# Kernel optimization log

Measured on AMD Instinct MI355X. Metric: run time of the kernel, lower is better.

## Reference

```python
import jax, jax.numpy as jnp
import numpy as np

NUM_HEADS = 8
SLOPE = 8.0  # relative_bias_slope
NEG_SLOPE = 0.2  # LeakyReLU


def _rel_coords_table(L):
    # RelativePosEmb: table is (n+1, n+1, 1) with n = L-1; row/col 0 are zeros
    n = L - 1
    coords = jnp.linspace(-SLOPE / 2, SLOPE / 2, n)
    rel = coords[None, :] - coords[:, None]  # [n, n]
    tab = jnp.sign(rel) * jnp.log2(jnp.abs(rel) + 1.0) / np.log2(SLOPE + 1.0)
    full = jnp.zeros((L, L), dtype=tab.dtype).at[1:, 1:].set(tab)
    return full[..., None]  # [L, L, 1]


def setup_inputs() -> dict:
    key = jax.random.key(0)
    ks = jax.random.split(key, 7)
    B, L, C, inter = 16, 1024, 512, 64
    x = jax.random.normal(ks[0], (B, L, C), dtype=jnp.float32)
    attn_mask = jax.random.randint(ks[1], (B, L - 1), 0, 2) > 0
    W_qkv = jax.random.normal(ks[2], (C, 3 * C), dtype=jnp.float32) * 0.02
    W1 = jax.random.normal(ks[3], (1, inter), dtype=jnp.float32) * 0.5
    b1 = jax.random.normal(ks[4], (inter,), dtype=jnp.float32) * 0.1
    W2 = jax.random.normal(ks[5], (inter, NUM_HEADS), dtype=jnp.float32) * 0.1
    W_out = jax.random.normal(ks[6], (C, C), dtype=jnp.float32) * 0.02
    return {"x": x, "attn_mask": attn_mask, "W_qkv": W_qkv, "W1": W1,
            "b1": b1, "W2": W2, "W_out": W_out}


def reference(x, attn_mask, W_qkv, W1, b1, W2, W_out):
    B, L, C = x.shape
    H = NUM_HEADS
    d = C // H
    # QKV projection (no bias)
    qkv = (x @ W_qkv).reshape(B, L, 3, H, d)
    q = qkv[:, :, 0].transpose(0, 2, 1, 3)  # [B,H,L,d]
    k = qkv[:, :, 1].transpose(0, 2, 1, 3)
    v = qkv[:, :, 2].transpose(0, 2, 1, 3)
    # relative position bias via tiny MLP: [L,L,1] -> [L,L,H]
    tab = _rel_coords_table(L)
    h = jax.nn.leaky_relu(tab @ W1 + b1, NEG_SLOPE)
    rel_bias = (h @ W2).transpose(2, 0, 1)[None]  # [1,H,L,L]
    # mask: prepend always-true column, broadcast over query dim
    m = jnp.concatenate([jnp.ones((B, 1), dtype=bool), attn_mask], axis=1)  # [B,L]
    bias = jnp.where(m[:, None, None, :], rel_bias, -jnp.inf)  # [B,H,L,L]
    # math SDPA: softmax(q k^T / sqrt(d) + bias) v
    scores = jnp.einsum('bhld,bhmd->bhlm', q, k) * (d ** -0.5) + bias
    attn = jax.nn.softmax(scores, axis=-1)
    out = jnp.einsum('bhlm,bhmd->bhld', attn, v)
    out = out.transpose(0, 2, 1, 3).reshape(B, L, C)
    return out @ W_out
```

## Files before the change

kernel.cpp:

```cpp
#include <hip/hip_runtime.h>
#include <hip/hip_bf16.h>

typedef short s16x8 __attribute__((ext_vector_type(8)));
typedef float f32x4 __attribute__((ext_vector_type(4)));
typedef float f32x16 __attribute__((ext_vector_type(16)));
typedef unsigned int u32;
typedef unsigned int u32x4 __attribute__((ext_vector_type(4)));
typedef unsigned short u16x4 __attribute__((ext_vector_type(4)));
typedef unsigned long long u64;

#define LOG2E 1.4426950408889634f
#define QSCALE 0.18033688011112042f
#define NEG_BIG -3.0e38f

#define PKS(dst, a, b) asm("v_cvt_pk_bf16_f32 %0, %1, %2" : "=v"(dst) : "v"(a), "v"(b))
#define SWP(x, y) asm("v_permlane32_swap_b32 %0, %1" : "+v"(x), "+v"(y))

__device__ __forceinline__ unsigned short f2b(float f) {
    unsigned int u = __float_as_uint(f);
    unsigned int r = (u + 0x7fffu + ((u >> 16) & 1u)) >> 16;
    return (unsigned short)r;
}

__device__ __forceinline__ void g2l16(const void* g, void* l) {
    __builtin_amdgcn_global_load_lds(
        (const __attribute__((address_space(1))) unsigned int*)(g),
        (__attribute__((address_space(3))) unsigned int*)(l), 16, 0, 0);
}

__global__ __launch_bounds__(256) void k_prepw(const float* __restrict__ Wqkv,
                                               unsigned short* __restrict__ wqkvT,
                                               const float* __restrict__ Wout,
                                               unsigned short* __restrict__ woutT,
                                               const float* __restrict__ W1,
                                               const float* __restrict__ b1,
                                               const float* __restrict__ W2,
                                               float* __restrict__ btab) {
    int bid = blockIdx.x, tid = threadIdx.x;
    {
        int idx = bid * 256 + tid;
        int k = idx & 511, n = idx >> 9;
        wqkvT[idx] = f2b(Wqkv[(long)k * 1536 + n]);
    }
    if (bid < 1024) {
        int idx = bid * 256 + tid;
        int k = idx & 511, n = idx >> 9;
        woutT[idx] = f2b(Wout[(long)k * 512 + n]);
    }
    if (bid >= 3064) {
        int idx = (bid - 3064) * 256 + tid;
        if (idx <= 2045) {
            float t = 0.0f;
            if (idx != 2045) {
                float r = (float)(idx - 1022) * (8.0f / 1022.0f);
                float sg = (r > 0.f) ? 1.0f : ((r < 0.f) ? -1.0f : 0.0f);
                t = sg * log2f(fabsf(r) + 1.0f) * 0.3154648767971406f;
            }
            float acc[8] = {0, 0, 0, 0, 0, 0, 0, 0};
            float accc[8] = {0, 0, 0, 0, 0, 0, 0, 0};
            for (int j = 0; j < 64; ++j) {
                float hj = t * W1[j] + b1[j];
                hj = (hj > 0.f) ? hj : 0.2f * hj;
                float hc = b1[j];
                hc = (hc > 0.f) ? hc : 0.2f * hc;
                #pragma unroll
                for (int h = 0; h < 8; ++h) {
                    acc[h] += hj * W2[j * 8 + h];
                    accc[h] += hc * W2[j * 8 + h];
                }
            }
            #pragma unroll
            for (int h = 0; h < 8; ++h) {
                btab[h * 4096 + idx] = acc[h] * LOG2E - 8.0f;
                btab[h * 4096 + 2048 + idx] = accc[h] * LOG2E - 8.0f;
            }
        }
    }
}

template <int MODE>
__global__ __launch_bounds__(256) void k_gemm(const float* __restrict__ Af,
                                              const unsigned short* __restrict__ A16,
                                              const unsigned short* __restrict__ BT,
                                              int M, int N,
                                              unsigned short* __restrict__ Qp,
                                              unsigned short* __restrict__ Kp,
                                              unsigned short* __restrict__ VTp,
                                              float* __restrict__ Cout) {
    __shared__ __align__(16) unsigned short As[2][128 * 32];
    __shared__ __align__(16) unsigned short Bs[2][128 * 32];
    constexpr int NX = (MODE == 0) ? 12 : 4;
    constexpr int NWG = (MODE == 0) ? 1536 : 512;
    int lid = blockIdx.y * NX + blockIdx.x;
    int tile = (lid & 7) * (NWG >> 3) + (lid >> 3);
    int m0 = (tile / NX) * 128, n0 = (tile % NX) * 128;
    int tid = threadIdx.x;
    int wave = tid >> 6, lane = tid & 63, lr = lane & 15, g = lane >> 4;
    int wr = wave >> 1, wc = wave & 1;
    f32x4 acc[4][4] = {};
    const float* Af0 = Af + (long)(m0 + (tid >> 2)) * 512 + (tid & 3) * 8;
    const float* Af1 = Af0 + 64 * 512;
    const char* Ab = (const char*)A16 + (long)(m0 + (tid >> 2)) * 1024 + (tid & 3) * 16;
    const char* Bb = (const char*)BT + (long)(n0 + (tid >> 2)) * 1024 + (tid & 3) * 16;

    if (MODE == 0) {
        f32x4 a0 = *(const f32x4*)(Af0);
        f32x4 a1 = *(const f32x4*)(Af0 + 4);
        f32x4 a2 = *(const f32x4*)(Af1);
        f32x4 a3 = *(const f32x4*)(Af1 + 4);
        u32 w0, w1, w2, w3;
        PKS(w0, a0.x, a0.y); PKS(w1, a0.z, a0.w);
        PKS(w2, a1.x, a1.y); PKS(w3, a1.z, a1.w);
        *(u32x4*)((char*)As[0] + tid * 16) = u32x4{w0, w1, w2, w3};
        PKS(w0, a2.x, a2.y); PKS(w1, a2.z, a2.w);
        PKS(w2, a3.x, a3.y); PKS(w3, a3.z, a3.w);
        *(u32x4*)((char*)As[0] + 4096 + tid * 16) = u32x4{w0, w1, w2, w3};
    } else {
        g2l16(Ab, (char*)As[0] + wave * 1024);
        g2l16(Ab + 65536, (char*)As[0] + 4096 + wave * 1024);
    }
    g2l16(Bb, (char*)Bs[0] + wave * 1024);
    g2l16(Bb + 65536, (char*)Bs[0] + 4096 + wave * 1024);
    __syncthreads();

    for (int kt = 0; kt < 16; ++kt) {
        int cur = kt & 1;
        int nxt = cur ^ 1;
        f32x4 na0, na1, na2, na3;
        if (kt < 15) {
            if (MODE == 0) {
                na0 = *(const f32x4*)(Af0 + (kt + 1) * 32);
                na1 = *(const f32x4*)(Af0 + (kt + 1) * 32 + 4);
                na2 = *(const f32x4*)(Af1 + (kt + 1) * 32);
                na3 = *(const f32x4*)(Af1 + (kt + 1) * 32 + 4);
            } else {
                g2l16(Ab + (kt + 1) * 64, (char*)As[nxt] + wave * 1024);
                g2l16(Ab + 65536 + (kt + 1) * 64, (char*)As[nxt] + 4096 + wave * 1024);
            }
            g2l16(Bb + (kt + 1) * 64, (char*)Bs[nxt] + wave * 1024);
            g2l16(Bb + 65536 + (kt + 1) * 64, (char*)Bs[nxt] + 4096 + wave * 1024);
        }
        s16x8 av[4], bv[4];
        #pragma unroll
        for (int f = 0; f < 4; ++f) {
            av[f] = *(const s16x8*)((char*)As[cur] + (wr * 64 + f * 16 + lr) * 64 + g * 16);
            bv[f] = *(const s16x8*)((char*)Bs[cur] + (wc * 64 + f * 16 + lr) * 64 + g * 16);
        }
        __builtin_amdgcn_s_setprio(1);
        #pragma unroll
        for (int fi = 0; fi < 4; ++fi)
            #pragma unroll
            for (int fj = 0; fj < 4; ++fj)
                acc[fi][fj] = __builtin_amdgcn_mfma_f32_16x16x32_bf16(bv[fj], av[fi], acc[fi][fj], 0, 0, 0);
        __builtin_amdgcn_s_setprio(0);
        if (MODE == 0 && kt < 15) {
            u32 w0, w1, w2, w3;
            PKS(w0, na0.x, na0.y); PKS(w1, na0.z, na0.w);
            PKS(w2, na1.x, na1.y); PKS(w3, na1.z, na1.w);
            *(u32x4*)((char*)As[nxt] + tid * 16) = u32x4{w0, w1, w2, w3};
            PKS(w0, na2.x, na2.y); PKS(w1, na2.z, na2.w);
            PKS(w2, na3.x, na3.y); PKS(w3, na3.z, na3.w);
            *(u32x4*)((char*)As[nxt] + 4096 + tid * 16) = u32x4{w0, w1, w2, w3};
        }
        __syncthreads();
    }
    #pragma unroll
    for (int fi = 0; fi < 4; ++fi) {
        int gm = m0 + wr * 64 + fi * 16 + lr;
        if (MODE == 0) {
            int bq = gm >> 10, lp = gm & 1023;
            int kvt = lp >> 6, kvl = lp & 63;
            #pragma unroll
            for (int fj = 0; fj < 4; ++fj) {
                int col0 = n0 + wc * 64 + fj * 16 + g * 4;
                int sec = col0 >> 9, c0 = col0 & 511, h = c0 >> 6, dd0 = c0 & 63;
                int bh = bq * 8 + h;
                float v0 = acc[fi][fj][0], v1 = acc[fi][fj][1];
                float v2 = acc[fi][fj][2], v3 = acc[fi][fj][3];
                if (sec == 0) {
                    u32 w0, w1;
                    float q0 = v0 * QSCALE, q1 = v1 * QSCALE, q2 = v2 * QSCALE, q3 = v3 * QSCALE;
                    PKS(w0, q0, q1); PKS(w1, q2, q3);
                    *(uint2*)(Qp + (long)(bh * 1024 + lp) * 64 + dd0) = make_uint2(w0, w1);
                } else if (sec == 1) {
                    u32 w0, w1;
                    PKS(w0, v0, v1); PKS(w1, v2, v3);
                    long off = (long)bh * 65536 + kvt * 4096 + (kvl >> 5) * 2048 +
                               (dd0 >> 4) * 512 + ((((dd0 >> 3) & 1) << 5) + (kvl & 31)) * 8 + (dd0 & 7);
                    *(uint2*)(Kp + off) = make_uint2(w0, w1);
                } else {
                    long off = (long)bh * 65536 + kvt * 4096 + (dd0 >> 5) * 2048 +
                               (kvl >> 4) * 512 + ((((kvl >> 3) & 1) << 5) + (dd0 & 31)) * 8 + (kvl & 7);
                    VTp[off] = f2b(v0);
                    VTp[off + 8] = f2b(v1);
                    VTp[off + 16] = f2b(v2);
                    VTp[off + 24] = f2b(v3);
                }
            }
        } else {
            #pragma unroll
            for (int fj = 0; fj < 4; ++fj) {
                int col0 = n0 + wc * 64 + fj * 16 + g * 4;
                *(f32x4*)(Cout + (long)gm * N + col0) = acc[fi][fj];
            }
        }
    }
}

#define ATT_STAGE(MTT) do { \
    char* Kn_ = smem + ((MTT) % 3) * 16384; \
    g2l16(Kg + (MTT) * 8192 + tid * 16, Kn_ + wave * 1024); \
    g2l16(Vg + (MTT) * 8192 + tid * 16, Kn_ + 8192 + wave * 1024); \
  } while (0)

#define ATT_PV(VPTR) do { \
    __builtin_amdgcn_s_setprio(1); \
    o0 = __builtin_amdgcn_mfma_f32_32x32x16_bf16(*(const s16x8*)((VPTR) + lx), Pc0, o0, 0, 0, 0); \
    o0 = __builtin_amdgcn_mfma_f32_32x32x16_bf16(*(const s16x8*)((VPTR) + 1024 + lx), Pc1, o0, 0, 0, 0); \
    o0 = __builtin_amdgcn_mfma_f32_32x32x16_bf16(*(const s16x8*)((VPTR) + 2048 + lx), Pc2, o0, 0, 0, 0); \
    o0 = __builtin_amdgcn_mfma_f32_32x32x16_bf16(*(const s16x8*)((VPTR) + 3072 + lx), Pc3, o0, 0, 0, 0); \
    o1 = __builtin_amdgcn_mfma_f32_32x32x16_bf16(*(const s16x8*)((VPTR) + 4096 + lx), Pc0, o1, 0, 0, 0); \
    o1 = __builtin_amdgcn_mfma_f32_32x32x16_bf16(*(const s16x8*)((VPTR) + 5120 + lx), Pc1, o1, 0, 0, 0); \
    o1 = __builtin_amdgcn_mfma_f32_32x32x16_bf16(*(const s16x8*)((VPTR) + 6144 + lx), Pc2, o1, 0, 0, 0); \
    o1 = __builtin_amdgcn_mfma_f32_32x32x16_bf16(*(const s16x8*)((VPTR) + 7168 + lx), Pc3, o1, 0, 0, 0); \
    __builtin_amdgcn_s_setprio(0); \
  } while (0)

#define ATT_ITER(MT) do { \
    if ((MT) + 1 < 16) ATT_STAGE((MT) + 1); \
    char* Kl = smem + ((MT) % 3) * 16384; \
    int ib = (MT) * 64 - l + 1022; \
    float b0[16], b1v[16]; \
    { \
        const float* bq = bp + ib + 4 * hi; \
        _Pragma("unroll") \
        for (int k = 0; k < 4; ++k) { \
            f32x4 va = *(const f32x4*)(bq + 8 * k); \
            f32x4 vb = *(const f32x4*)(bq + 32 + 8 * k); \
            b0[4 * k + 0] = va.x; b0[4 * k + 1] = va.y; \
            b0[4 * k + 2] = va.z; b0[4 * k + 3] = va.w; \
            b1v[4 * k + 0] = vb.x; b1v[4 * k + 1] = vb.y; \
            b1v[4 * k + 2] = vb.z; b1v[4 * k + 3] = vb.w; \
        } \
    } \
    f32x16 s0 = {}, s1 = {}; \
    __builtin_amdgcn_s_setprio(1); \
    s0 = __builtin_amdgcn_mfma_f32_32x32x16_bf16(*(const s16x8*)(Kl + lx), qf0, s0, 0, 0, 0); \
    s0 = __builtin_amdgcn_mfma_f32_32x32x16_bf16(*(const s16x8*)(Kl + 1024 + lx), qf1, s0, 0, 0, 0); \
    s0 = __builtin_amdgcn_mfma_f32_32x32x16_bf16(*(const s16x8*)(Kl + 2048 + lx), qf2, s0, 0, 0, 0); \
    s0 = __builtin_amdgcn_mfma_f32_32x32x16_bf16(*(const s16x8*)(Kl + 3072 + lx), qf3, s0, 0, 0, 0); \
    s1 = __builtin_amdgcn_mfma_f32_32x32x16_bf16(*(const s16x8*)(Kl + 4096 + lx), qf0, s1, 0, 0, 0); \
    s1 = __builtin_amdgcn_mfma_f32_32x32x16_bf16(*(const s16x8*)(Kl + 5120 + lx), qf1, s1, 0, 0, 0); \
    s1 = __builtin_amdgcn_mfma_f32_32x32x16_bf16(*(const s16x8*)(Kl + 6144 + lx), qf2, s1, 0, 0, 0); \
    s1 = __builtin_amdgcn_mfma_f32_32x32x16_bf16(*(const s16x8*)(Kl + 7168 + lx), qf3, s1, 0, 0, 0); \
    __builtin_amdgcn_s_setprio(0); \
    if ((MT) > 0) { \
        char* Vp = smem + (((MT) + 2) % 3) * 16384 + 8192; \
        ATT_PV(Vp); \
    } \
    u64 mb = *(const u64*)(smem + 49152 + (MT) * 8); \
    u32 wm0 = (u32)(mb >> (4 * hi)); \
    u32 wm1 = (u32)(mb >> (32 + 4 * hi)); \
    if ((MT) == 0 && hi == 0) b0[0] = c2; \
    _Pragma("unroll") \
    for (int r = 0; r < 16; ++r) { \
        int pos = (r & 3) + 8 * (r >> 2); \
        s0[r] = ((wm0 >> pos) & 1) ? s0[r] + b0[r] : NEG_BIG; \
        s1[r] = ((wm1 >> pos) & 1) ? s1[r] + b1v[r] : NEG_BIG; \
    } \
    _Pragma("unroll") \
    for (int r = 0; r < 16; ++r) s0[r] = __builtin_amdgcn_exp2f(s0[r]); \
    _Pragma("unroll") \
    for (int r = 0; r < 16; ++r) s1[r] = __builtin_amdgcn_exp2f(s1[r]); \
    { \
        float u0 = s0[0] + s0[1], u1 = s0[2] + s0[3], u2 = s0[4] + s0[5], u3 = s0[6] + s0[7]; \
        float u4 = s0[8] + s0[9], u5 = s0[10] + s0[11], u6 = s0[12] + s0[13], u7 = s0[14] + s0[15]; \
        float v0 = s1[0] + s1[1], v1 = s1[2] + s1[3], v2 = s1[4] + s1[5], v3 = s1[6] + s1[7]; \
        float v4 = s1[8] + s1[9], v5 = s1[10] + s1[11], v6 = s1[12] + s1[13], v7 = s1[14] + s1[15]; \
        u0 += u1; u2 += u3; u4 += u5; u6 += u7; \
        v0 += v1; v2 += v3; v4 += v5; v6 += v7; \
        u0 += u2; u4 += u6; v0 += v2; v4 += v6; \
        float ts = (u0 + u4) + (v0 + v4); \
        ts += __shfl_xor(ts, 32); \
        Ss += ts; \
    } \
    { \
        u32 x, y, x2, y2; \
        union { u32 w[4]; s16x8 v; } pt; \
        PKS(x, s0[0], s0[1]);  PKS(y, s0[4], s0[5]);  SWP(x, y); \
        PKS(x2, s0[2], s0[3]); PKS(y2, s0[6], s0[7]); SWP(x2, y2); \
        pt.w[0] = x; pt.w[1] = x2; pt.w[2] = y; pt.w[3] = y2; Pc0 = pt.v; \
        PKS(x, s0[8], s0[9]);   PKS(y, s0[12], s0[13]);  SWP(x, y); \
        PKS(x2, s0[10], s0[11]); PKS(y2, s0[14], s0[15]); SWP(x2, y2); \
        pt.w[0] = x; pt.w[1] = x2; pt.w[2] = y; pt.w[3] = y2; Pc1 = pt.v; \
        PKS(x, s1[0], s1[1]);  PKS(y, s1[4], s1[5]);  SWP(x, y); \
        PKS(x2, s1[2], s1[3]); PKS(y2, s1[6], s1[7]); SWP(x2, y2); \
        pt.w[0] = x; pt.w[1] = x2; pt.w[2] = y; pt.w[3] = y2; Pc2 = pt.v; \
        PKS(x, s1[8], s1[9]);   PKS(y, s1[12], s1[13]);  SWP(x, y); \
        PKS(x2, s1[10], s1[11]); PKS(y2, s1[14], s1[15]); SWP(x2, y2); \
        pt.w[0] = x; pt.w[1] = x2; pt.w[2] = y; pt.w[3] = y2; Pc3 = pt.v; \
    } \
    __syncthreads(); \
  } while (0)

__global__ __launch_bounds__(512, 2) void k_attn(const unsigned short* __restrict__ Q,
                                                 const unsigned short* __restrict__ Kb,
                                                 const unsigned short* __restrict__ VT,
                                                 const int* __restrict__ mask,
                                                 const float* __restrict__ btab,
                                                 unsigned short* __restrict__ AO) {
    __shared__ __align__(16) char smem[56320];
    int lid = blockIdx.x;
    int wg = (lid & 7) * 64 + (lid >> 3);
    int qt = wg & 3, bh = wg >> 2;
    int b = bh >> 3, h = bh & 7;
    int tid = threadIdx.x;
    int wave = tid >> 6, lane = tid & 63;
    int q = lane & 31, hi = lane >> 5;
    int l = qt * 256 + wave * 32 + q;
    const float* bt = btab + h * 4096;
    float c2 = bt[2045];
    const float* bp = bt + ((l == 0) ? 2048 : 0);

    const char* Kg = (const char*)Kb + (long)bh * 131072;
    const char* Vg = (const char*)VT + (long)bh * 131072;

    if (tid < 16) {
        const int* mrow = mask + b * 1023;
        u64 bits = 0;
        for (int j = 0; j < 64; ++j) {
            int kv = tid * 64 + j;
            int bit = (kv == 0) ? 1 : (mrow[kv - 1] != 0);
            bits |= (u64)bit << j;
        }
        *(u64*)(smem + 49152 + tid * 8) = bits;
    }

    const char* Qrow = (const char*)Q + ((long)bh * 1024 + l) * 128;
    s16x8 qf0 = *(const s16x8*)(Qrow + 0 * 32 + hi * 16);
    s16x8 qf1 = *(const s16x8*)(Qrow + 1 * 32 + hi * 16);
    s16x8 qf2 = *(const s16x8*)(Qrow + 2 * 32 + hi * 16);
    s16x8 qf3 = *(const s16x8*)(Qrow + 3 * 32 + hi * 16);

    f32x16 o0 = {}, o1 = {};
    float Ss = 0.f;
    int lx = lane * 16;
    s16x8 Pc0 = {}, Pc1 = {}, Pc2 = {}, Pc3 = {};

    ATT_STAGE(0);
    __syncthreads();

    ATT_ITER(0);  ATT_ITER(1);  ATT_ITER(2);  ATT_ITER(3);
    ATT_ITER(4);  ATT_ITER(5);  ATT_ITER(6);  ATT_ITER(7);
    ATT_ITER(8);  ATT_ITER(9);  ATT_ITER(10); ATT_ITER(11);
    ATT_ITER(12); ATT_ITER(13); ATT_ITER(14); ATT_ITER(15);

    {
        char* Vp = smem + 0 * 16384 + 8192;
        ATT_PV(Vp);
    }
    __syncthreads();

    float inv = 1.0f / Ss;
    char* Ob = smem;
    int qloc = wave * 32 + q;
    #pragma unroll
    for (int j = 0; j < 4; ++j) {
        u32 wa, wb;
        float va0 = o0[j * 4 + 0] * inv, va1 = o0[j * 4 + 1] * inv;
        float va2 = o0[j * 4 + 2] * inv, va3 = o0[j * 4 + 3] * inv;
        PKS(wa, va0, va1); PKS(wb, va2, va3);
        int d0 = 8 * j + 4 * hi;
        *(uint2*)(Ob + qloc * 128 + ((d0 * 2) ^ ((qloc & 7) << 4))) = make_uint2(wa, wb);
    }
    #pragma unroll
    for (int j = 0; j < 4; ++j) {
        u32 wa, wb;
        float va0 = o1[j * 4 + 0] * inv, va1 = o1[j * 4 + 1] * inv;
        float va2 = o1[j * 4 + 2] * inv, va3 = o1[j * 4 + 3] * inv;
        PKS(wa, va0, va1); PKS(wb, va2, va3);
        int d0 = 32 + 8 * j + 4 * hi;
        *(uint2*)(Ob + qloc * 128 + ((d0 * 2) ^ ((qloc & 7) << 4))) = make_uint2(wa, wb);
    }
    __syncthreads();
    long gb = (long)(b * 1024 + qt * 256) * 512 + h * 64;
    #pragma unroll
    for (int p = 0; p < 4; ++p) {
        int qr = p * 64 + (tid >> 3);
        int ss = tid & 7;
        u32x4 vv = *(const u32x4*)(Ob + qr * 128 + ((ss * 16) ^ ((qr & 7) << 4)));
        *(u32x4*)((char*)AO + (gb + (long)qr * 512 + ss * 8) * 2) = vv;
    }
}


extern "C" void kernel_launch(void* const* d_in, const int* in_sizes, int n_in,
                              void* d_out, int out_size, void* d_ws, size_t ws_size,
                              hipStream_t stream) {
    const float* x    = (const float*)d_in[0];
    const int*   mask = (const int*)d_in[1];
    const float* Wqkv = (const float*)d_in[2];
    const float* W1   = (const float*)d_in[3];
    const float* b1   = (const float*)d_in[4];
    const float* W2   = (const float*)d_in[5];
    const float* Wout = (const float*)d_in[6];
    float* out = (float*)d_out;
    char* ws = (char*)d_ws;

    unsigned short* wqkvT = (unsigned short*)(ws + 16777216);
    unsigned short* woutT = (unsigned short*)(ws + 18350080);
    unsigned short* Qb    = (unsigned short*)(ws + 18874368);
    unsigned short* Kb    = (unsigned short*)(ws + 35651584);
    unsigned short* VTb   = (unsigned short*)(ws + 52428800);
    unsigned short* AOb   = (unsigned short*)(ws + 69206016);
    float* btab           = (float*)(ws + 85983232);
    if (ws_size < 86114304) return;

    k_prepw<<<3072, 256, 0, stream>>>(Wqkv, wqkvT, Wout, woutT, W1, b1, W2, btab);
    k_gemm<0><<<dim3(12, 128), 256, 0, stream>>>(x, nullptr, wqkvT, 16384, 1536, Qb, Kb, VTb, nullptr);
    k_attn<<<512, 512, 0, stream>>>(Qb, Kb, VTb, mask, btab, AOb);
    k_gemm<1><<<dim3(4, 128), 256, 0, stream>>>(nullptr, AOb, woutT, 16384, 512, nullptr, nullptr, nullptr, out);
}
```

Baseline: 142.5 us.

## Software-pipeline attention loop: overlap next-tile QK MFMA with previous tile softmax

Restructures the attention inner loop so the QK^T MFMAs for tile MT are issued before the softmax, bias/mask and PV of tile MT-1, using double-buffered score registers (sA/sB). The aim is to hide the exp2/bias/pack VALU work behind matrix-core work from the next tile instead of serializing QK then softmax within each iteration. It adds two more 16-wide f32 register arrays, which raises register pressure at launch bounds 512x2 and could cause spills. The 3-stage LDS buffer must still hold V of tile MT-1 while K of MT+1 is loaded.

```diff
diff --git a/kernel.cpp b/kernel.cpp
--- a/kernel.cpp
+++ b/kernel.cpp
@@ -213,6 +213,23 @@
     g2l16(Vg + (MTT) * 8192 + tid * 16, Kn_ + 8192 + wave * 1024); \
   } while (0)
 
+#define ATT_QK(MT, S0, S1) do { \
+    if ((MT) + 1 < 16) ATT_STAGE((MT) + 1); \
+    char* Kl = smem + ((MT) % 3) * 16384; \
+    f32x16 t0_ = {}, t1_ = {}; \
+    __builtin_amdgcn_s_setprio(1); \
+    t0_ = __builtin_amdgcn_mfma_f32_32x32x16_bf16(*(const s16x8*)(Kl + lx), qf0, t0_, 0, 0, 0); \
+    t0_ = __builtin_amdgcn_mfma_f32_32x32x16_bf16(*(const s16x8*)(Kl + 1024 + lx), qf1, t0_, 0, 0, 0); \
+    t0_ = __builtin_amdgcn_mfma_f32_32x32x16_bf16(*(const s16x8*)(Kl + 2048 + lx), qf2, t0_, 0, 0, 0); \
+    t0_ = __builtin_amdgcn_mfma_f32_32x32x16_bf16(*(const s16x8*)(Kl + 3072 + lx), qf3, t0_, 0, 0, 0); \
+    t1_ = __builtin_amdgcn_mfma_f32_32x32x16_bf16(*(const s16x8*)(Kl + 4096 + lx), qf0, t1_, 0, 0, 0); \
+    t1_ = __builtin_amdgcn_mfma_f32_32x32x16_bf16(*(const s16x8*)(Kl + 5120 + lx), qf1, t1_, 0, 0, 0); \
+    t1_ = __builtin_amdgcn_mfma_f32_32x32x16_bf16(*(const s16x8*)(Kl + 6144 + lx), qf2, t1_, 0, 0, 0); \
+    t1_ = __builtin_amdgcn_mfma_f32_32x32x16_bf16(*(const s16x8*)(Kl + 7168 + lx), qf3, t1_, 0, 0, 0); \
+    __builtin_amdgcn_s_setprio(0); \
+    S0 = t0_; S1 = t1_; \
+  } while (0)
+
 #define ATT_PV(VPTR) do { \
     __builtin_amdgcn_s_setprio(1); \
     o0 = __builtin_amdgcn_mfma_f32_32x32x16_bf16(*(const s16x8*)((VPTR) + lx), Pc0, o0, 0, 0, 0); \
@@ -226,10 +243,8 @@
     __builtin_amdgcn_s_setprio(0); \
   } while (0)
 
-#define ATT_ITER(MT) do { \
-    if ((MT) + 1 < 16) ATT_STAGE((MT) + 1); \
-    char* Kl = smem + ((MT) % 3) * 16384; \
-    int ib = (MT) * 64 - l + 1022; \
+#define ATT_SM(MTP, S0, S1) do { \
+    int ib = (MTP) * 64 - l + 1022; \
     float b0[16], b1v[16]; \
     { \
         const float* bq = bp + ib + 4 * hi; \
@@ -243,40 +258,25 @@
             b1v[4 * k + 2] = vb.z; b1v[4 * k + 3] = vb.w; \
         } \
     } \
-    f32x16 s0 = {}, s1 = {}; \
-    __builtin_amdgcn_s_setprio(1); \
-    s0 = __builtin_amdgcn_mfma_f32_32x32x16_bf16(*(const s16x8*)(Kl + lx), qf0, s0, 0, 0, 0); \
-    s0 = __builtin_amdgcn_mfma_f32_32x32x16_bf16(*(const s16x8*)(Kl + 1024 + lx), qf1, s0, 0, 0, 0); \
-    s0 = __builtin_amdgcn_mfma_f32_32x32x16_bf16(*(const s16x8*)(Kl + 2048 + lx), qf2, s0, 0, 0, 0); \
-    s0 = __builtin_amdgcn_mfma_f32_32x32x16_bf16(*(const s16x8*)(Kl + 3072 + lx), qf3, s0, 0, 0, 0); \
-    s1 = __builtin_amdgcn_mfma_f32_32x32x16_bf16(*(const s16x8*)(Kl + 4096 + lx), qf0, s1, 0, 0, 0); \
-    s1 = __builtin_amdgcn_mfma_f32_32x32x16_bf16(*(const s16x8*)(Kl + 5120 + lx), qf1, s1, 0, 0, 0); \
-    s1 = __builtin_amdgcn_mfma_f32_32x32x16_bf16(*(const s16x8*)(Kl + 6144 + lx), qf2, s1, 0, 0, 0); \
-    s1 = __builtin_amdgcn_mfma_f32_32x32x16_bf16(*(const s16x8*)(Kl + 7168 + lx), qf3, s1, 0, 0, 0); \
-    __builtin_amdgcn_s_setprio(0); \
-    if ((MT) > 0) { \
-        char* Vp = smem + (((MT) + 2) % 3) * 16384 + 8192; \
-        ATT_PV(Vp); \
-    } \
-    u64 mb = *(const u64*)(smem + 49152 + (MT) * 8); \
+    u64 mb = *(const u64*)(smem + 49152 + (MTP) * 8); \
     u32 wm0 = (u32)(mb >> (4 * hi)); \
     u32 wm1 = (u32)(mb >> (32 + 4 * hi)); \
-    if ((MT) == 0 && hi == 0) b0[0] = c2; \
+    if ((MTP) == 0 && hi == 0) b0[0] = c2; \
     _Pragma("unroll") \
     for (int r = 0; r < 16; ++r) { \
         int pos = (r & 3) + 8 * (r >> 2); \
-        s0[r] = ((wm0 >> pos) & 1) ? s0[r] + b0[r] : NEG_BIG; \
-        s1[r] = ((wm1 >> pos) & 1) ? s1[r] + b1v[r] : NEG_BIG; \
+        S0[r] = ((wm0 >> pos) & 1) ? S0[r] + b0[r] : NEG_BIG; \
+        S1[r] = ((wm1 >> pos) & 1) ? S1[r] + b1v[r] : NEG_BIG; \
     } \
     _Pragma("unroll") \
-    for (int r = 0; r < 16; ++r) s0[r] = __builtin_amdgcn_exp2f(s0[r]); \
+    for (int r = 0; r < 16; ++r) S0[r] = __builtin_amdgcn_exp2f(S0[r]); \
     _Pragma("unroll") \
-    for (int r = 0; r < 16; ++r) s1[r] = __builtin_amdgcn_exp2f(s1[r]); \
+    for (int r = 0; r < 16; ++r) S1[r] = __builtin_amdgcn_exp2f(S1[r]); \
     { \
-        float u0 = s0[0] + s0[1], u1 = s0[2] + s0[3], u2 = s0[4] + s0[5], u3 = s0[6] + s0[7]; \
-        float u4 = s0[8] + s0[9], u5 = s0[10] + s0[11], u6 = s0[12] + s0[13], u7 = s0[14] + s0[15]; \
-        float v0 = s1[0] + s1[1], v1 = s1[2] + s1[3], v2 = s1[4] + s1[5], v3 = s1[6] + s1[7]; \
-        float v4 = s1[8] + s1[9], v5 = s1[10] + s1[11], v6 = s1[12] + s1[13], v7 = s1[14] + s1[15]; \
+        float u0 = S0[0] + S0[1], u1 = S0[2] + S0[3], u2 = S0[4] + S0[5], u3 = S0[6] + S0[7]; \
+        float u4 = S0[8] + S0[9], u5 = S0[10] + S0[11], u6 = S0[12] + S0[13], u7 = S0[14] + S0[15]; \
+        float v0 = S1[0] + S1[1], v1 = S1[2] + S1[3], v2 = S1[4] + S1[5], v3 = S1[6] + S1[7]; \
+        float v4 = S1[8] + S1[9], v5 = S1[10] + S1[11], v6 = S1[12] + S1[13], v7 = S1[14] + S1[15]; \
         u0 += u1; u2 += u3; u4 += u5; u6 += u7; \
         v0 += v1; v2 += v3; v4 += v5; v6 += v7; \
         u0 += u2; u4 += u6; v0 += v2; v4 += v6; \
@@ -287,19 +287,28 @@
     { \
         u32 x, y, x2, y2; \
         union { u32 w[4]; s16x8 v; } pt; \
-        PKS(x, s0[0], s0[1]);  PKS(y, s0[4], s0[5]);  SWP(x, y); \
-        PKS(x2, s0[2], s0[3]); PKS(y2, s0[6], s0[7]); SWP(x2, y2); \
+        PKS(x, S0[0], S0[1]);  PKS(y, S0[4], S0[5]);  SWP(x, y); \
+        PKS(x2, S0[2], S0[3]); PKS(y2, S0[6], S0[7]); SWP(x2, y2); \
         pt.w[0] = x; pt.w[1] = x2; pt.w[2] = y; pt.w[3] = y2; Pc0 = pt.v; \
-        PKS(x, s0[8], s0[9]);   PKS(y, s0[12], s0[13]);  SWP(x, y); \
-        PKS(x2, s0[10], s0[11]); PKS(y2, s0[14], s0[15]); SWP(x2, y2); \
+        PKS(x, S0[8], S0[9]);   PKS(y, S0[12], S0[13]);  SWP(x, y); \
+        PKS(x2, S0[10], S0[11]); PKS(y2, S0[14], S0[15]); SWP(x2, y2); \
         pt.w[0] = x; pt.w[1] = x2; pt.w[2] = y; pt.w[3] = y2; Pc1 = pt.v; \
-        PKS(x, s1[0], s1[1]);  PKS(y, s1[4], s1[5]);  SWP(x, y); \
-        PKS(x2, s1[2], s1[3]); PKS(y2, s1[6], s1[7]); SWP(x2, y2); \
+        PKS(x, S1[0], S1[1]);  PKS(y, S1[4], S1[5]);  SWP(x, y); \
+        PKS(x2, S1[2], S1[3]); PKS(y2, S1[6], S1[7]); SWP(x2, y2); \
         pt.w[0] = x; pt.w[1] = x2; pt.w[2] = y; pt.w[3] = y2; Pc2 = pt.v; \
-        PKS(x, s1[8], s1[9]);   PKS(y, s1[12], s1[13]);  SWP(x, y); \
-        PKS(x2, s1[10], s1[11]); PKS(y2, s1[14], s1[15]); SWP(x2, y2); \
+        PKS(x, S1[8], S1[9]);   PKS(y, S1[12], S1[13]);  SWP(x, y); \
+        PKS(x2, S1[10], S1[11]); PKS(y2, S1[14], S1[15]); SWP(x2, y2); \
         pt.w[0] = x; pt.w[1] = x2; pt.w[2] = y; pt.w[3] = y2; Pc3 = pt.v; \
     } \
+    { \
+        char* Vp_ = smem + ((MTP) % 3) * 16384 + 8192; \
+        ATT_PV(Vp_); \
+    } \
+  } while (0)
+
+#define ATT_IT(MT, SC0, SC1, SP0, SP1) do { \
+    ATT_QK(MT, SC0, SC1); \
+    ATT_SM((MT) - 1, SP0, SP1); \
     __syncthreads(); \
   } while (0)
 
@@ -346,19 +355,24 @@
     float Ss = 0.f;
     int lx = lane * 16;
     s16x8 Pc0 = {}, Pc1 = {}, Pc2 = {}, Pc3 = {};
+    f32x16 sA0, sA1, sB0, sB1;
 
     ATT_STAGE(0);
     __syncthreads();
 
-    ATT_ITER(0);  ATT_ITER(1);  ATT_ITER(2);  ATT_ITER(3);
-    ATT_ITER(4);  ATT_ITER(5);  ATT_ITER(6);  ATT_ITER(7);
-    ATT_ITER(8);  ATT_ITER(9);  ATT_ITER(10); ATT_ITER(11);
-    ATT_ITER(12); ATT_ITER(13); ATT_ITER(14); ATT_ITER(15);
-
-    {
-        char* Vp = smem + 0 * 16384 + 8192;
-        ATT_PV(Vp);
-    }
+    ATT_QK(0, sA0, sA1);
+    __syncthreads();
+
+    ATT_IT(1, sB0, sB1, sA0, sA1);   ATT_IT(2, sA0, sA1, sB0, sB1);
+    ATT_IT(3, sB0, sB1, sA0, sA1);   ATT_IT(4, sA0, sA1, sB0, sB1);
+    ATT_IT(5, sB0, sB1, sA0, sA1);   ATT_IT(6, sA0, sA1, sB0, sB1);
+    ATT_IT(7, sB0, sB1, sA0, sA1);   ATT_IT(8, sA0, sA1, sB0, sB1);
+    ATT_IT(9, sB0, sB1, sA0, sA1);   ATT_IT(10, sA0, sA1, sB0, sB1);
+    ATT_IT(11, sB0, sB1, sA0, sA1);  ATT_IT(12, sA0, sA1, sB0, sB1);
+    ATT_IT(13, sB0, sB1, sA0, sA1);  ATT_IT(14, sA0, sA1, sB0, sB1);
+    ATT_IT(15, sB0, sB1, sA0, sA1);
+
+    ATT_SM(15, sB0, sB1);
     __syncthreads();
 
     float inv = 1.0f / Ss;
```

Result: slower. 148.8 us (+4.5%).
